# Optimization experiments

Measured on AMD Instinct MI355X. Metric: run time of the kernel, lower is better.

The kernel has to match this reference:

```python
import jax, jax.numpy as jnp
import numpy as np

# Static problem sizes (batch 'batch' vector is built as B equal-sized graphs).
B, N_PER, K = 4, 4096, 64          # graphs, points per graph, max_num_neighbors
RATIO, R = 0.25, 0.2               # fps ratio, radius
M = int(N_PER * RATIO)             # fps samples per graph (1024)
C_IN = 64                          # input feature channels
MLP_DIMS = [C_IN + 3, 64, 64, 128]


def setup_inputs() -> dict:
    key = jax.random.key(0)
    ks = jax.random.split(key, 8)
    x = jax.random.normal(ks[0], (B * N_PER, C_IN), dtype=jnp.float32)
    pos = jax.random.uniform(ks[1], (B * N_PER, 3), dtype=jnp.float32)
    batch = jnp.repeat(jnp.arange(B, dtype=jnp.int32), N_PER)

    def lin(k, fan_in, fan_out):
        s = 1.0 / np.sqrt(fan_in)
        return jax.random.uniform(k, (fan_in, fan_out), jnp.float32, -s, s)

    W1 = lin(ks[2], MLP_DIMS[0], MLP_DIMS[1]); b1 = jnp.zeros((MLP_DIMS[1],), jnp.float32)
    W2 = lin(ks[3], MLP_DIMS[1], MLP_DIMS[2]); b2 = jnp.zeros((MLP_DIMS[2],), jnp.float32)
    W3 = lin(ks[4], MLP_DIMS[2], MLP_DIMS[3]); b3 = jnp.zeros((MLP_DIMS[3],), jnp.float32)
    return {"x": x, "pos": pos, "batch": batch,
            "W1": W1, "b1": b1, "W2": W2, "b2": b2, "W3": W3, "b3": b3}


def _fps(pos_b):
    """Farthest point sampling on one graph. pos_b: [n,3] -> [M] int32 indices.
    Deterministic start at index 0 (PyG uses a random start)."""
    n = pos_b.shape[0]

    def step(carry, _):
        dists, last = carry
        d = jnp.sum((pos_b - pos_b[last]) ** 2, axis=-1)
        dists = jnp.minimum(dists, d)
        nxt = jnp.argmax(dists).astype(jnp.int32)
        return (dists, nxt), nxt

    init = (jnp.full((n,), jnp.inf, dtype=pos_b.dtype), jnp.int32(0))
    _, rest = jax.lax.scan(step, init, None, length=M - 1)
    return jnp.concatenate([jnp.zeros((1,), jnp.int32), rest])


def _radius(pos_b):
    """Radius neighbor search (self-query). Returns nbr [n,K] indices and valid [n,K] mask.
    Takes the K nearest in-ball neighbors (self always included, d=0)."""
    d2 = jnp.sum((pos_b[:, None, :] - pos_b[None, :, :]) ** 2, axis=-1)  # [n,n]
    neg = jnp.where(d2 <= R * R, -d2, -jnp.inf)
    vals, nbr = jax.lax.top_k(neg, K)
    return nbr, vals > -jnp.inf


def _pointconv(x_b, pos_b, nbr, valid, W1, b1, W2, b2, W3, b3):
    """PointConv: out_i = max_{j in N(i)} MLP(concat(x_j, pos_j - pos_i))."""
    rel = pos_b[nbr] - pos_b[:, None, :]                 # [n,K,3]
    feat = jnp.concatenate([x_b[nbr], rel], axis=-1)     # [n,K,C_IN+3]
    h = jax.nn.relu(feat @ W1 + b1)
    h = jax.nn.relu(h @ W2 + b2)
    h = jax.nn.relu(h @ W3 + b3)                          # [n,K,128]
    h = jnp.where(valid[..., None], h, -jnp.inf)          # mask padded neighbor slots
    return h.max(axis=1)                                  # [n,128]; self-edge guarantees validity


def reference(x, pos, batch, W1, b1, W2, b2, W3, b3):
    xb = x.reshape(B, N_PER, C_IN)
    pb = pos.reshape(B, N_PER, 3)
    nbr, valid = jax.vmap(_radius)(pb)                    # [B,n,K]
    out = jax.vmap(_pointconv, in_axes=(0, 0, 0, 0) + (None,) * 6)(
        xb, pb, nbr, valid, W1, b1, W2, b2, W3, b3)       # [B,n,128]
    idx = jax.vmap(_fps)(pb)                              # [B,M]
    x_s = jnp.take_along_axis(out, idx[..., None], axis=1).reshape(B * M, -1)
    pos_s = jnp.take_along_axis(pb, idx[..., None], axis=1).reshape(B * M, 3)
    batch_s = jnp.repeat(jnp.arange(B, dtype=batch.dtype), M)
    return x_s, pos_s, batch_s
```

## Files before the change

kernel.cpp:

```cpp
#include <hip/hip_runtime.h>

#define NPER 4096
#define MS   1024
#define CIN  64
#define LCAP 384

typedef float  f32x4 __attribute__((ext_vector_type(4)));
typedef short  s16x8 __attribute__((ext_vector_type(8)));

__device__ __forceinline__ float d2_exact(float ax, float ay, float az,
                                          float bx, float by, float bz) {
  float dx = __fsub_rn(ax, bx);
  float dy = __fsub_rn(ay, by);
  float dz = __fsub_rn(az, bz);
  return __fadd_rn(__fadd_rn(__fmul_rn(dx, dx), __fmul_rn(dy, dy)), __fmul_rn(dz, dz));
}

__device__ __forceinline__ unsigned short f2bf(float f) {
  unsigned b = __float_as_uint(f);
  return (unsigned short)((b + 0x7FFFu + ((b >> 16) & 1u)) >> 16);
}

template <int CTRL, int RMASK>
__device__ __forceinline__ unsigned long long dpp_max_step(unsigned long long k) {
  int hi = (int)(unsigned)(k >> 32);
  int lo = (int)(unsigned)(k & 0xFFFFFFFFull);
  int thi = __builtin_amdgcn_update_dpp(hi, hi, CTRL, RMASK, 0xF, false);
  int tlo = __builtin_amdgcn_update_dpp(lo, lo, CTRL, RMASK, 0xF, false);
  unsigned long long t =
      ((unsigned long long)(unsigned)thi << 32) | (unsigned)tlo;
  return t > k ? t : k;
}

__device__ __forceinline__ unsigned long long u64max(unsigned long long a,
                                                    unsigned long long b) {
  return a > b ? a : b;
}

__global__ __launch_bounds__(256) void fps_kernel(const float* __restrict__ pos,
                                                  int* __restrict__ idx_out) {
  const int b = blockIdx.x;
  const int t = threadIdx.x;
  __shared__ float4 s_pos4[NPER];
  __shared__ __align__(16) unsigned long long s_red[2][4];
  const float* pb = pos + (size_t)b * NPER * 3;
  for (int i = t; i < NPER; i += 256)
    s_pos4[i] = make_float4(pb[i * 3], pb[i * 3 + 1], pb[i * 3 + 2], 0.f);
  if (t == 0) idx_out[b * MS] = 0;
  __syncthreads();

  float px[16], py[16], pz[16], dist[16];
#pragma unroll
  for (int j = 0; j < 16; ++j) {
    float4 p = s_pos4[t + j * 256];
    px[j] = p.x; py[j] = p.y; pz[j] = p.z;
    dist[j] = __builtin_inff();
  }
  const int w = t >> 6, lane = t & 63;
  float sx = s_pos4[0].x, sy = s_pos4[0].y, sz = s_pos4[0].z;

  for (int m = 1; m < MS; ++m) {
    float bd0 = -1.f, bd1 = -1.f, bd2 = -1.f, bd3 = -1.f;
    int bi0 = 0, bi1 = 0, bi2 = 0, bi3 = 0;
#pragma unroll
    for (int k = 0; k < 4; ++k) {
      {
        const int j = k;
        float d2 = d2_exact(px[j], py[j], pz[j], sx, sy, sz);
        float nd = fminf(dist[j], d2);
        dist[j] = nd;
        if (nd > bd0) { bd0 = nd; bi0 = t + j * 256; }
      }
      {
        const int j = 4 + k;
        float d2 = d2_exact(px[j], py[j], pz[j], sx, sy, sz);
        float nd = fminf(dist[j], d2);
        dist[j] = nd;
        if (nd > bd1) { bd1 = nd; bi1 = t + j * 256; }
      }
      {
        const int j = 8 + k;
        float d2 = d2_exact(px[j], py[j], pz[j], sx, sy, sz);
        float nd = fminf(dist[j], d2);
        dist[j] = nd;
        if (nd > bd2) { bd2 = nd; bi2 = t + j * 256; }
      }
      {
        const int j = 12 + k;
        float d2 = d2_exact(px[j], py[j], pz[j], sx, sy, sz);
        float nd = fminf(dist[j], d2);
        dist[j] = nd;
        if (nd > bd3) { bd3 = nd; bi3 = t + j * 256; }
      }
    }
    if (bd1 > bd0) { bd0 = bd1; bi0 = bi1; }
    if (bd3 > bd2) { bd2 = bd3; bi2 = bi3; }
    if (bd2 > bd0) { bd0 = bd2; bi0 = bi2; }

    unsigned long long k =
        ((unsigned long long)__float_as_uint(bd0) << 32) | (unsigned)(~bi0);
    k = dpp_max_step<0x111, 0xF>(k);
    k = dpp_max_step<0x112, 0xF>(k);
    k = dpp_max_step<0x114, 0xF>(k);
    k = dpp_max_step<0x118, 0xF>(k);
    k = dpp_max_step<0x142, 0xA>(k);
    k = dpp_max_step<0x143, 0xC>(k);
    const int par = m & 1;
    if (lane == 63) s_red[par][w] = k;
    __syncthreads();
    ulonglong2 ab = *reinterpret_cast<const ulonglong2*>(&s_red[par][0]);
    ulonglong2 cd = *reinterpret_cast<const ulonglong2*>(&s_red[par][2]);
    unsigned long long kb = u64max(u64max(ab.x, ab.y), u64max(cd.x, cd.y));
    const int nx = (int)(~(unsigned)(kb & 0xFFFFFFFFull));
    if (t == 0) idx_out[b * MS + m] = nx;
    float4 wp = s_pos4[nx];
    sx = wp.x; sy = wp.y; sz = wp.z;
  }
}

__global__ __launch_bounds__(512, 4) void radconv_kernel(
    const float* __restrict__ x, const float* __restrict__ pos,
    const int* __restrict__ idx,
    const float* __restrict__ W1, const float* __restrict__ B1,
    const float* __restrict__ W2, const float* __restrict__ B2,
    const float* __restrict__ W3, const float* __restrict__ B3,
    float* __restrict__ out) {
  const int t = threadIdx.x;
  const int g = blockIdx.x >> 9;
  const int qpair = blockIdx.x & 511;
  const float* pb = pos + (size_t)g * NPER * 3;
  const float* xb = x + (size_t)g * NPER * CIN;

  __shared__ int s_cnt[2];
  __shared__ float s_ctr[2][4];
  __shared__ __align__(16) unsigned long long s_list[2][LCAP];
  __shared__ int s_nbr[2][64];
  __shared__ __align__(16) unsigned short sFeat[2][64 * 104];
  __shared__ __align__(16) unsigned short sW1[64 * 104];
  __shared__ __align__(16) unsigned short sW2[64 * 72];
  __shared__ __align__(16) unsigned short sW3[128 * 72];

  if (t < 2) s_cnt[t] = 0;
  const int q0 = g * MS + qpair * 2;
  const int qiA = idx[q0], qiB = idx[q0 + 1];
  const float cAx = pb[qiA * 3], cAy = pb[qiA * 3 + 1], cAz = pb[qiA * 3 + 2];
  const float cBx = pb[qiB * 3], cBy = pb[qiB * 3 + 1], cBz = pb[qiB * 3 + 2];
  if (t == 0) { s_ctr[0][0] = cAx; s_ctr[0][1] = cAy; s_ctr[0][2] = cAz; }
  if (t == 1) { s_ctr[1][0] = cBx; s_ctr[1][1] = cBy; s_ctr[1][2] = cBz; }
  __syncthreads();

  {
    float pp[24];
    const float4* pv = (const float4*)(pb + (size_t)t * 24);
#pragma unroll
    for (int r = 0; r < 6; ++r) {
      float4 v = pv[r];
      pp[r * 4 + 0] = v.x; pp[r * 4 + 1] = v.y;
      pp[r * 4 + 2] = v.z; pp[r * 4 + 3] = v.w;
    }
#pragma unroll
    for (int jj = 0; jj < 8; ++jj) {
      const int j = t * 8 + jj;
      const float X = pp[jj * 3], Y = pp[jj * 3 + 1], Z = pp[jj * 3 + 2];
      float dA = d2_exact(X, Y, Z, cAx, cAy, cAz);
      if (dA <= 0.04f) {
        int p = atomicAdd(&s_cnt[0], 1);
        if (p < LCAP)
          s_list[0][p] = ((unsigned long long)__float_as_uint(dA) << 32) | (unsigned)j;
      }
      float dB = d2_exact(X, Y, Z, cBx, cBy, cBz);
      if (dB <= 0.04f) {
        int p = atomicAdd(&s_cnt[1], 1);
        if (p < LCAP)
          s_list[1][p] = ((unsigned long long)__float_as_uint(dB) << 32) | (unsigned)j;
      }
    }
  }
  for (int ee = t; ee < 64 * 64; ee += 512) {
    int c = ee >> 6, kk = 67 + (ee & 63);
    if (kk < 104) sW1[c * 104 + kk] = 0;
  }
  for (int e = t; e < 67 * 64; e += 512) {
    int k = e >> 6, c = e & 63;
    sW1[c * 104 + k] = f2bf(W1[e]);
  }
  for (int e = t; e < 64 * 64; e += 512) {
    int k = e >> 6, c = e & 63;
    sW2[c * 72 + k] = f2bf(W2[e]);
  }
  for (int e = t; e < 64 * 128; e += 512) {
    int k = e >> 7, c = e & 127;
    sW3[c * 72 + k] = f2bf(W3[e]);
  }
  __syncthreads();

  const int w = t >> 6, lane = t & 63;
  const int c0 = min(min(s_cnt[0], LCAP), 64);
  const int c1 = min(min(s_cnt[1], LCAP), 64);

  {
    const int rq = w >> 2;
    const int nsurv = min(s_cnt[rq], LCAP);
    for (int e = (w & 3) * 64 + lane; e < nsurv; e += 256) {
      unsigned long long mykey = s_list[rq][e];
      int rank = 0;
      int o = 0;
      for (; o + 8 <= nsurv; o += 8) {
        unsigned long long k0 = s_list[rq][o + 0], k1 = s_list[rq][o + 1];
        unsigned long long k2 = s_list[rq][o + 2], k3 = s_list[rq][o + 3];
        unsigned long long k4 = s_list[rq][o + 4], k5 = s_list[rq][o + 5];
        unsigned long long k6 = s_list[rq][o + 6], k7 = s_list[rq][o + 7];
        rank += (k0 < mykey) + (k1 < mykey) + (k2 < mykey) + (k3 < mykey) +
                (k4 < mykey) + (k5 < mykey) + (k6 < mykey) + (k7 < mykey);
      }
      for (; o < nsurv; ++o) rank += (s_list[rq][o] < mykey) ? 1 : 0;
      if (rank < 64) s_nbr[rq][rank] = (int)(mykey & 0xFFFFFFFFull);
    }
  }
  __syncthreads();

  {
    const int slot = t >> 2, part = t & 3;
    const int gq = slot >> 6, s = slot & 63;
    const int cq = gq ? c1 : c0;
    unsigned short* frow = &sFeat[gq][s * 104];
    uint4 z; z.x = z.y = z.z = z.w = 0u;
    if (s < cq) {
      const int j = s_nbr[gq][s];
      const float4* xr = (const float4*)(xb + (size_t)j * CIN + part * 16);
      float4 v0 = xr[0], v1 = xr[1], v2 = xr[2], v3 = xr[3];
      uint4 w0, w1;
      w0.x = f2bf(v0.x) | ((unsigned)f2bf(v0.y) << 16);
      w0.y = f2bf(v0.z) | ((unsigned)f2bf(v0.w) << 16);
      w0.z = f2bf(v1.x) | ((unsigned)f2bf(v1.y) << 16);
      w0.w = f2bf(v1.z) | ((unsigned)f2bf(v1.w) << 16);
      w1.x = f2bf(v2.x) | ((unsigned)f2bf(v2.y) << 16);
      w1.y = f2bf(v2.z) | ((unsigned)f2bf(v2.w) << 16);
      w1.z = f2bf(v3.x) | ((unsigned)f2bf(v3.y) << 16);
      w1.w = f2bf(v3.z) | ((unsigned)f2bf(v3.w) << 16);
      *(uint4*)(frow + part * 16) = w0;
      *(uint4*)(frow + part * 16 + 8) = w1;
      uint4 rz = z;
      if (part == 0) {
        const float cx = gq ? cBx : cAx, cy = gq ? cBy : cAy, cz = gq ? cBz : cAz;
        rz.x = f2bf(pb[j * 3] - cx) | ((unsigned)f2bf(pb[j * 3 + 1] - cy) << 16);
        rz.y = (unsigned)f2bf(pb[j * 3 + 2] - cz);
      }
      *(uint4*)(frow + 64 + part * 8) = rz;
    } else {
      *(uint4*)(frow + part * 16) = z;
      *(uint4*)(frow + part * 16 + 8) = z;
      *(uint4*)(frow + 64 + part * 8) = z;
    }
  }
  __syncthreads();

  const int qq2 = w >> 2;
  const int mt = w & 3;
  const int lo = lane & 15, hi = lane >> 4;
  unsigned short* F = &sFeat[qq2][0];
  const int arow = (16 * mt + lo) * 104;
  const int hrow = (16 * mt + hi * 4) * 104;

  {
    f32x4 acc[4];
#pragma unroll
    for (int n = 0; n < 4; ++n) {
      float bb = B1[n * 16 + lo];
      acc[n] = (f32x4){bb, bb, bb, bb};
    }
    s16x8 a0 = *(const s16x8*)(F + arow + 0 + hi * 8);
    s16x8 a1 = *(const s16x8*)(F + arow + 32 + hi * 8);
    s16x8 a2 = *(const s16x8*)(F + arow + 64 + hi * 8);
#pragma unroll
    for (int n = 0; n < 4; ++n) {
      const unsigned short* Bp = &sW1[(n * 16 + lo) * 104 + hi * 8];
      s16x8 b0 = *(const s16x8*)(Bp);
      s16x8 b1 = *(const s16x8*)(Bp + 32);
      s16x8 b2 = *(const s16x8*)(Bp + 64);
      acc[n] = __builtin_amdgcn_mfma_f32_16x16x32_bf16(a0, b0, acc[n], 0, 0, 0);
      acc[n] = __builtin_amdgcn_mfma_f32_16x16x32_bf16(a1, b1, acc[n], 0, 0, 0);
      acc[n] = __builtin_amdgcn_mfma_f32_16x16x32_bf16(a2, b2, acc[n], 0, 0, 0);
    }
#pragma unroll
    for (int n = 0; n < 4; ++n)
#pragma unroll
      for (int r = 0; r < 4; ++r)
        F[hrow + r * 104 + n * 16 + lo] = f2bf(fmaxf(acc[n][r], 0.f));
  }
  {
    f32x4 acc[4];
#pragma unroll
    for (int n = 0; n < 4; ++n) {
      float bb = B2[n * 16 + lo];
      acc[n] = (f32x4){bb, bb, bb, bb};
    }
    s16x8 a0 = *(const s16x8*)(F + arow + 0 + hi * 8);
    s16x8 a1 = *(const s16x8*)(F + arow + 32 + hi * 8);
#pragma unroll
    for (int n = 0; n < 4; ++n) {
      const unsigned short* Bp = &sW2[(n * 16 + lo) * 72 + hi * 8];
      s16x8 b0 = *(const s16x8*)(Bp);
      s16x8 b1 = *(const s16x8*)(Bp + 32);
      acc[n] = __builtin_amdgcn_mfma_f32_16x16x32_bf16(a0, b0, acc[n], 0, 0, 0);
      acc[n] = __builtin_amdgcn_mfma_f32_16x16x32_bf16(a1, b1, acc[n], 0, 0, 0);
    }
#pragma unroll
    for (int n = 0; n < 4; ++n)
#pragma unroll
      for (int r = 0; r < 4; ++r)
        F[hrow + r * 104 + n * 16 + lo] = f2bf(fmaxf(acc[n][r], 0.f));
  }
  float pm[8];
  {
    const int cq = qq2 ? c1 : c0;
    f32x4 acc[8];
#pragma unroll
    for (int n = 0; n < 8; ++n) {
      float bb = B3[n * 16 + lo];
      acc[n] = (f32x4){bb, bb, bb, bb};
    }
    s16x8 a0 = *(const s16x8*)(F + arow + 0 + hi * 8);
    s16x8 a1 = *(const s16x8*)(F + arow + 32 + hi * 8);
#pragma unroll
    for (int n = 0; n < 8; ++n) {
      const unsigned short* Bp = &sW3[(n * 16 + lo) * 72 + hi * 8];
      s16x8 b0 = *(const s16x8*)(Bp);
      s16x8 b1 = *(const s16x8*)(Bp + 32);
      acc[n] = __builtin_amdgcn_mfma_f32_16x16x32_bf16(a0, b0, acc[n], 0, 0, 0);
      acc[n] = __builtin_amdgcn_mfma_f32_16x16x32_bf16(a1, b1, acc[n], 0, 0, 0);
    }
#pragma unroll
    for (int n = 0; n < 8; ++n) {
      float v = -1e30f;
#pragma unroll
      for (int r = 0; r < 4; ++r) {
        int row = 16 * mt + hi * 4 + r;
        if (row < cq) v = fmaxf(v, fmaxf(acc[n][r], 0.f));
      }
      pm[n] = v;
    }
  }
  __syncthreads();

  float* red = (float*)&sFeat[0][0];
#pragma unroll
  for (int n = 0; n < 8; ++n)
    red[((qq2 * 128) + n * 16 + lo) * 17 + mt * 4 + hi] = pm[n];
  __syncthreads();

  if (t < 256) {
    const int gq = t >> 7, cc = t & 127;
    const float* rp = red + (gq * 128 + cc) * 17;
    float v = rp[0];
#pragma unroll
    for (int p = 1; p < 16; ++p) v = fmaxf(v, rp[p]);
    out[(size_t)(q0 + gq) * 128 + cc] = v;
  }
  if (t == 256 || t == 257) {
    const int gq = t - 256;
    const int qrow = q0 + gq;
    out[524288 + qrow * 3 + 0] = s_ctr[gq][0];
    out[524288 + qrow * 3 + 1] = s_ctr[gq][1];
    out[524288 + qrow * 3 + 2] = s_ctr[gq][2];
    out[536576 + qrow] = (float)g;
  }
}

extern "C" void kernel_launch(void* const* d_in, const int* in_sizes, int n_in,
                              void* d_out, int out_size, void* d_ws, size_t ws_size,
                              hipStream_t stream) {
  const float* x   = (const float*)d_in[0];
  const float* pos = (const float*)d_in[1];
  const float* W1  = (const float*)d_in[3];
  const float* B1  = (const float*)d_in[4];
  const float* W2  = (const float*)d_in[5];
  const float* B2  = (const float*)d_in[6];
  const float* W3  = (const float*)d_in[7];
  const float* B3  = (const float*)d_in[8];
  float* out = (float*)d_out;
  int* idx = (int*)d_ws;

  fps_kernel<<<4, 256, 0, stream>>>(pos, idx);
  radconv_kernel<<<2048, 512, 0, stream>>>(x, pos, idx, W1, B1, W2, B2, W3, B3, out);
}
```

Baseline: 681.8 us.

## Speculatively emit two FPS samples per round via top-2 reduction

New measurement: 822.2 us. +20.6%, slower.

```diff
diff --git a/kernel.cpp b/kernel.cpp
--- a/kernel.cpp
+++ b/kernel.cpp
@@ -7,6 +7,7 @@
 
 typedef float  f32x4 __attribute__((ext_vector_type(4)));
 typedef short  s16x8 __attribute__((ext_vector_type(8)));
+typedef unsigned long long u64;
 
 __device__ __forceinline__ float d2_exact(float ax, float ay, float az,
                                           float bx, float by, float bz) {
@@ -21,20 +22,29 @@
   return (unsigned short)((b + 0x7FFFu + ((b >> 16) & 1u)) >> 16);
 }
 
-template <int CTRL, int RMASK>
-__device__ __forceinline__ unsigned long long dpp_max_step(unsigned long long k) {
-  int hi = (int)(unsigned)(k >> 32);
-  int lo = (int)(unsigned)(k & 0xFFFFFFFFull);
-  int thi = __builtin_amdgcn_update_dpp(hi, hi, CTRL, RMASK, 0xF, false);
-  int tlo = __builtin_amdgcn_update_dpp(lo, lo, CTRL, RMASK, 0xF, false);
-  unsigned long long t =
-      ((unsigned long long)(unsigned)thi << 32) | (unsigned)tlo;
-  return t > k ? t : k;
-}
-
-__device__ __forceinline__ unsigned long long u64max(unsigned long long a,
-                                                    unsigned long long b) {
-  return a > b ? a : b;
+__device__ __forceinline__ u64 mk64(unsigned hi, unsigned lo) {
+  return ((u64)hi << 32) | lo;
+}
+
+__device__ __forceinline__ void top2_merge(u64& a1, u64& a2, u64 o1, u64 o2) {
+  bool g = a1 > o1;
+  u64 n1 = g ? a1 : o1;
+  u64 mn = g ? o1 : a1;
+  u64 mx = (a2 > o2) ? a2 : o2;
+  a2 = (mn > mx) ? mn : mx;
+  a1 = n1;
+}
+
+template <int CTRL, int RMASK, bool BC>
+__device__ __forceinline__ void dpp_top2_step(u64& b1, u64& b2) {
+  int a1hi = (int)(unsigned)(b1 >> 32), a1lo = (int)(unsigned)(b1 & 0xFFFFFFFFull);
+  int a2hi = (int)(unsigned)(b2 >> 32), a2lo = (int)(unsigned)(b2 & 0xFFFFFFFFull);
+  int o1hi = __builtin_amdgcn_update_dpp(a1hi, a1hi, CTRL, RMASK, 0xF, BC);
+  int o1lo = __builtin_amdgcn_update_dpp(a1lo, a1lo, CTRL, RMASK, 0xF, BC);
+  int o2hi = __builtin_amdgcn_update_dpp(a2hi, a2hi, CTRL, RMASK, 0xF, BC);
+  int o2lo = __builtin_amdgcn_update_dpp(a2lo, a2lo, CTRL, RMASK, 0xF, BC);
+  top2_merge(b1, b2, mk64((unsigned)o1hi, (unsigned)o1lo),
+             mk64((unsigned)o2hi, (unsigned)o2lo));
 }
 
 __global__ __launch_bounds__(256) void fps_kernel(const float* __restrict__ pos,
@@ -42,7 +52,7 @@
   const int b = blockIdx.x;
   const int t = threadIdx.x;
   __shared__ float4 s_pos4[NPER];
-  __shared__ __align__(16) unsigned long long s_red[2][4];
+  __shared__ __align__(16) u64 s_red[2][8];
   const float* pb = pos + (size_t)b * NPER * 3;
   for (int i = t; i < NPER; i += 256)
     s_pos4[i] = make_float4(pb[i * 3], pb[i * 3 + 1], pb[i * 3 + 2], 0.f);
@@ -50,71 +60,80 @@
   __syncthreads();
 
   float px[16], py[16], pz[16], dist[16];
+  unsigned lo16[16];
 #pragma unroll
   for (int j = 0; j < 16; ++j) {
     float4 p = s_pos4[t + j * 256];
     px[j] = p.x; py[j] = p.y; pz[j] = p.z;
     dist[j] = __builtin_inff();
+    lo16[j] = ~(unsigned)(t + j * 256);
   }
   const int w = t >> 6, lane = t & 63;
-  float sx = s_pos4[0].x, sy = s_pos4[0].y, sz = s_pos4[0].z;
-
-  for (int m = 1; m < MS; ++m) {
-    float bd0 = -1.f, bd1 = -1.f, bd2 = -1.f, bd3 = -1.f;
-    int bi0 = 0, bi1 = 0, bi2 = 0, bi3 = 0;
-#pragma unroll
-    for (int k = 0; k < 4; ++k) {
-      {
-        const int j = k;
-        float d2 = d2_exact(px[j], py[j], pz[j], sx, sy, sz);
-        float nd = fminf(dist[j], d2);
+  float wxa[2], wya[2], wza[2];
+  wxa[0] = s_pos4[0].x; wya[0] = s_pos4[0].y; wza[0] = s_pos4[0].z;
+  int npend = 1, nout = 1, rnd = 0;
+
+  while (nout < MS) {
+    u64 b1 = 0, b2 = 0;
+    if (npend == 2) {
+#pragma unroll
+      for (int j = 0; j < 16; ++j) {
+        float nd = dist[j];
+        nd = fminf(nd, d2_exact(px[j], py[j], pz[j], wxa[0], wya[0], wza[0]));
+        nd = fminf(nd, d2_exact(px[j], py[j], pz[j], wxa[1], wya[1], wza[1]));
         dist[j] = nd;
-        if (nd > bd0) { bd0 = nd; bi0 = t + j * 256; }
-      }
-      {
-        const int j = 4 + k;
-        float d2 = d2_exact(px[j], py[j], pz[j], sx, sy, sz);
-        float nd = fminf(dist[j], d2);
+        u64 kj = mk64(__float_as_uint(nd), lo16[j]);
+        bool g = kj > b1;
+        u64 b2c = g ? b1 : kj;
+        b1 = g ? kj : b1;
+        b2 = (b2c > b2) ? b2c : b2;
+      }
+    } else {
+#pragma unroll
+      for (int j = 0; j < 16; ++j) {
+        float nd = dist[j];
+        nd = fminf(nd, d2_exact(px[j], py[j], pz[j], wxa[0], wya[0], wza[0]));
         dist[j] = nd;
-        if (nd > bd1) { bd1 = nd; bi1 = t + j * 256; }
-      }
-      {
-        const int j = 8 + k;
-        float d2 = d2_exact(px[j], py[j], pz[j], sx, sy, sz);
-        float nd = fminf(dist[j], d2);
-        dist[j] = nd;
-        if (nd > bd2) { bd2 = nd; bi2 = t + j * 256; }
-      }
-      {
-        const int j = 12 + k;
-        float d2 = d2_exact(px[j], py[j], pz[j], sx, sy, sz);
-        float nd = fminf(dist[j], d2);
-        dist[j] = nd;
-        if (nd > bd3) { bd3 = nd; bi3 = t + j * 256; }
-      }
-    }
-    if (bd1 > bd0) { bd0 = bd1; bi0 = bi1; }
-    if (bd3 > bd2) { bd2 = bd3; bi2 = bi3; }
-    if (bd2 > bd0) { bd0 = bd2; bi0 = bi2; }
-
-    unsigned long long k =
-        ((unsigned long long)__float_as_uint(bd0) << 32) | (unsigned)(~bi0);
-    k = dpp_max_step<0x111, 0xF>(k);
-    k = dpp_max_step<0x112, 0xF>(k);
-    k = dpp_max_step<0x114, 0xF>(k);
-    k = dpp_max_step<0x118, 0xF>(k);
-    k = dpp_max_step<0x142, 0xA>(k);
-    k = dpp_max_step<0x143, 0xC>(k);
-    const int par = m & 1;
-    if (lane == 63) s_red[par][w] = k;
+        u64 kj = mk64(__float_as_uint(nd), lo16[j]);
+        bool g = kj > b1;
+        u64 b2c = g ? b1 : kj;
+        b1 = g ? kj : b1;
+        b2 = (b2c > b2) ? b2c : b2;
+      }
+    }
+    dpp_top2_step<0x111, 0xF, true>(b1, b2);
+    dpp_top2_step<0x112, 0xF, true>(b1, b2);
+    dpp_top2_step<0x114, 0xF, true>(b1, b2);
+    dpp_top2_step<0x118, 0xF, true>(b1, b2);
+    dpp_top2_step<0x142, 0xA, false>(b1, b2);
+    dpp_top2_step<0x143, 0xC, false>(b1, b2);
+    const int par = rnd & 1;
+    if (lane == 63) { s_red[par][2 * w] = b1; s_red[par][2 * w + 1] = b2; }
     __syncthreads();
-    ulonglong2 ab = *reinterpret_cast<const ulonglong2*>(&s_red[par][0]);
-    ulonglong2 cd = *reinterpret_cast<const ulonglong2*>(&s_red[par][2]);
-    unsigned long long kb = u64max(u64max(ab.x, ab.y), u64max(cd.x, cd.y));
-    const int nx = (int)(~(unsigned)(kb & 0xFFFFFFFFull));
-    if (t == 0) idx_out[b * MS + m] = nx;
-    float4 wp = s_pos4[nx];
-    sx = wp.x; sy = wp.y; sz = wp.z;
+    ulonglong2 q0 = *(const ulonglong2*)&s_red[par][0];
+    ulonglong2 q1 = *(const ulonglong2*)&s_red[par][2];
+    ulonglong2 q2 = *(const ulonglong2*)&s_red[par][4];
+    ulonglong2 q3 = *(const ulonglong2*)&s_red[par][6];
+    u64 K1 = q0.x, K2 = q0.y;
+    top2_merge(K1, K2, q1.x, q1.y);
+    top2_merge(K1, K2, q2.x, q2.y);
+    top2_merge(K1, K2, q3.x, q3.y);
+    const unsigned i1 = ~(unsigned)(K1 & 0xFFFFFFFFull);
+    const unsigned i2 = ~(unsigned)(K2 & 0xFFFFFFFFull);
+    float4 wp1 = s_pos4[i1];
+    float4 wp2 = s_pos4[i2];
+    float sd = d2_exact(wp2.x, wp2.y, wp2.z, wp1.x, wp1.y, wp1.z);
+    float k2d = __uint_as_float((unsigned)(K2 >> 32));
+    const bool spec = (sd >= k2d) && (nout <= MS - 2);
+    if (t == 0) {
+      idx_out[b * MS + nout] = (int)i1;
+      if (spec) idx_out[b * MS + nout + 1] = (int)i2;
+    }
+    wxa[0] = wp1.x; wya[0] = wp1.y; wza[0] = wp1.z;
+    wxa[1] = wp2.x; wya[1] = wp2.y; wza[1] = wp2.z;
+    npend = spec ? 2 : 1;
+    nout += spec ? 2 : 1;
+    rnd++;
   }
 }
 
```
